# Optimization experiments

Hardware: AMD Instinct MI355X
Metric: run time of the kernel (lower is better)

The kernel has to match this reference:

```python
import jax, jax.numpy as jnp
import numpy as np

B, N = 16384, 64

def setup_inputs() -> dict:
    key = jax.random.key(0)
    a = jax.random.normal(key, (B, N, N), dtype=jnp.float32)
    # symeig / eigh require symmetric input; symmetrize like SPD inputs would be
    x = 0.5 * (a + jnp.swapaxes(a, -2, -1))
    return {"input": x}

def reference(input) -> jnp.ndarray:
    # s, u = symeig(input); out = u @ diag(exp(s)) @ u^T
    s, u = jnp.linalg.eigh(input)          # s: [B,N], u: [B,N,N]
    # fuse diag_embed + two matmuls: (u * exp(s)) @ u^T
    return jnp.einsum('bik,bk,bjk->bij', u, jnp.exp(s), u)
```

## Files before the change

### kernel.cpp

```cpp
#include <hip/hip_runtime.h>
#include <math.h>

#define NB 64
#define TPB 256

__device__ __constant__ float CF[16] = {
    1.0f,
    1.0f,
    0.5f,
    1.6666666666666666e-01f,
    4.1666666666666664e-02f,
    8.3333333333333332e-03f,
    1.3888888888888889e-03f,
    1.9841269841269841e-04f,
    2.4801587301587302e-05f,
    2.7557319223985893e-06f,
    2.7557319223985888e-07f,
    2.5052108385441720e-08f,
    2.0876756987868100e-09f,
    1.6059043836821613e-10f,
    1.1470745597729725e-11f,
    7.6471637318198164e-13f
};

typedef __attribute__((ext_vector_type(8))) short bf16x8;
typedef __attribute__((ext_vector_type(16))) float f32x16;
typedef __attribute__((ext_vector_type(4))) unsigned int u32x4;

#define MFMA32 __builtin_amdgcn_mfma_f32_32x32x16_bf16

__device__ __forceinline__ void split_pk(float x0, float x1, unsigned& ph, unsigned& pl) {
    unsigned h;
    asm("v_cvt_pk_bf16_f32 %0, %1, %2" : "=v"(h) : "v"(x0), "v"(x1));
    float h0 = __builtin_bit_cast(float, h << 16);
    float h1 = __builtin_bit_cast(float, h & 0xFFFF0000u);
    float r0 = x0 - h0;
    float r1 = x1 - h1;
    unsigned l;
    asm("v_cvt_pk_bf16_f32 %0, %1, %2" : "=v"(l) : "v"(r0), "v"(r1));
    ph = h; pl = l;
}

__device__ __forceinline__ float bf2f(unsigned short h) {
    unsigned u = ((unsigned)h) << 16;
    return __builtin_bit_cast(float, u);
}

__device__ __forceinline__ unsigned swzoff(int row, int byteInRow) {
    return (unsigned)(row * 128 + (byteInRow ^ ((row & 7) << 4)));
}

__device__ __forceinline__ bf16x8 ldfrag(const unsigned short* buf, int row, int f, int lh) {
    const char* p = (const char*)buf + swzoff(row, f * 32 + lh * 16);
    return __builtin_bit_cast(bf16x8, *(const u32x4*)p);
}

__device__ __forceinline__ f32x16 mm3(const bf16x8* ah, const bf16x8* al,
                                      const bf16x8* bh, const bf16x8* bl) {
    f32x16 acc = {};
#pragma unroll
    for (int f = 0; f < 4; ++f) acc = MFMA32(ah[f], bh[f], acc, 0, 0, 0);
#pragma unroll
    for (int f = 0; f < 4; ++f) acc = MFMA32(al[f], bh[f], acc, 0, 0, 0);
#pragma unroll
    for (int f = 0; f < 4; ++f) acc = MFMA32(ah[f], bl[f], acc, 0, 0, 0);
    return acc;
}

__device__ __forceinline__ void store_cT(unsigned short* Bh, unsigned short* Bl,
                                         const float* v, int c_out, int rbase) {
#pragma unroll
    for (int g = 0; g < 4; ++g) {
        uint2 wh, wl;
        split_pk(v[g * 4 + 0], v[g * 4 + 1], wh.x, wl.x);
        split_pk(v[g * 4 + 2], v[g * 4 + 3], wh.y, wl.y);
        unsigned off = swzoff(c_out, (rbase + g * 8) * 2);
        *(uint2*)((char*)Bh + off) = wh;
        *(uint2*)((char*)Bl + off) = wl;
    }
}

__global__ __launch_bounds__(TPB, 4)
void spd_expmap_mfma(const float* __restrict__ in, float* __restrict__ out)
{
    __shared__ __align__(16) unsigned short SB[2 * 4096];
    __shared__ float fscratch[4];
    unsigned short* Bh = SB;
    unsigned short* Bl = SB + 4096;

    const int tid  = threadIdx.x;
    const int lane = tid & 63;
    const int wv   = tid >> 6;
    const int wr   = (wv >> 1) * 32;
    const int wc   = (wv & 1) * 32;
    const int l31  = lane & 31;
    const int lh   = lane >> 5;
    const int c_out = wc + l31;
    const int rbase = wr + 4 * lh;
    const size_t base = (size_t)blockIdx.x * (NB * NB);
    const bool diag = (wr == wc);

    float dsel[16];
#pragma unroll
    for (int g = 0; g < 4; ++g)
#pragma unroll
        for (int q = 0; q < 4; ++q)
            dsel[g * 4 + q] = (rbase + g * 8 + q == c_out) ? 1.0f : 0.0f;

    {
        const int r  = tid >> 2;
        const int cb = (tid & 3) * 16;
        const float4* gp = (const float4*)(in + base) + tid * 4;
        float vv[16];
#pragma unroll
        for (int i = 0; i < 4; ++i) {
            float4 t = gp[i];
            vv[i * 4 + 0] = t.x; vv[i * 4 + 1] = t.y;
            vv[i * 4 + 2] = t.z; vv[i * 4 + 3] = t.w;
        }
        unsigned hw[8], lw[8];
#pragma unroll
        for (int i = 0; i < 8; ++i)
            split_pk(vv[2 * i], vv[2 * i + 1], hw[i], lw[i]);
        u32x4 H0 = {hw[0], hw[1], hw[2], hw[3]}, H1 = {hw[4], hw[5], hw[6], hw[7]};
        u32x4 L0 = {lw[0], lw[1], lw[2], lw[3]}, L1 = {lw[4], lw[5], lw[6], lw[7]};
        unsigned o0 = swzoff(r, cb * 2), o1 = swzoff(r, cb * 2 + 16);
        *(u32x4*)((char*)Bh + o0) = H0; *(u32x4*)((char*)Bh + o1) = H1;
        *(u32x4*)((char*)Bl + o0) = L0; *(u32x4*)((char*)Bl + o1) = L1;
    }
    __syncthreads();

    f32x16 acc;
    {
        bf16x8 ah[4], al[4], bh[4], bl[4];
#pragma unroll
        for (int f = 0; f < 4; ++f) {
            ah[f] = ldfrag(Bh, wr + l31, f, lh);
            al[f] = ldfrag(Bl, wr + l31, f, lh);
        }
        if (diag) {
#pragma unroll
            for (int f = 0; f < 4; ++f) { bh[f] = ah[f]; bl[f] = al[f]; }
        } else {
#pragma unroll
            for (int f = 0; f < 4; ++f) {
                bh[f] = ldfrag(Bh, wc + l31, f, lh);
                bl[f] = ldfrag(Bl, wc + l31, f, lh);
            }
        }
        acc = mm3(ah, al, bh, bl);
        float fr = 0.f;
#pragma unroll
        for (int r = 0; r < 16; ++r) fr += acc[r] * acc[r];
#pragma unroll
        for (int off = 32; off; off >>= 1) fr += __shfl_xor(fr, off);
        if (lane == 0) fscratch[wv] = fr;
    }

    float x_out[16];
#pragma unroll
    for (int g = 0; g < 4; ++g) {
        unsigned off = swzoff(c_out, (rbase + g * 8) * 2);
        uint2 xh = *(const uint2*)((const char*)Bh + off);
        uint2 xl = *(const uint2*)((const char*)Bl + off);
        x_out[g * 4 + 0] = bf2f((unsigned short)(xh.x & 0xFFFF)) + bf2f((unsigned short)(xl.x & 0xFFFF));
        x_out[g * 4 + 1] = bf2f((unsigned short)(xh.x >> 16))    + bf2f((unsigned short)(xl.x >> 16));
        x_out[g * 4 + 2] = bf2f((unsigned short)(xh.y & 0xFFFF)) + bf2f((unsigned short)(xl.y & 0xFFFF));
        x_out[g * 4 + 3] = bf2f((unsigned short)(xh.y >> 16))    + bf2f((unsigned short)(xl.y >> 16));
    }
    __syncthreads();

    const float total = fscratch[0] + fscratch[1] + fscratch[2] + fscratch[3];
    const float bound = sqrtf(sqrtf(total));
    int sexp = 0;
    if (bound > 4.f) {
        sexp = (int)ceilf(log2f(bound)) - 2;
        if (sexp < 0) sexp = 0;
        if (sexp > 24) sexp = 24;
    }
    const float sc1 = exp2f(-(float)sexp);
    const float sc2 = sc1 * sc1;
#pragma unroll
    for (int r = 0; r < 16; ++r) x_out[r] *= sc1;

    {
        float v[16];
#pragma unroll
        for (int r = 0; r < 16; ++r) v[r] = acc[r] * sc2;
        store_cT(Bh, Bl, v, c_out, rbase);
    }
    __syncthreads();

    bf16x8 ya_h[4], ya_l[4];
#pragma unroll
    for (int f = 0; f < 4; ++f) {
        ya_h[f] = ldfrag(Bh, wr + l31, f, lh);
        ya_l[f] = ldfrag(Bl, wr + l31, f, lh);
    }
    __syncthreads();

    {
        float v[16];
#pragma unroll
        for (int r = 0; r < 16; ++r)
            v[r] = fmaf(dsel[r], CF[12], CF[13] * x_out[r]);
        store_cT(Bh, Bl, v, c_out, rbase);
    }
    __syncthreads();

#pragma unroll 1
    for (int j = 5; j >= 0; --j) {
        bf16x8 pbh[4], pbl[4];
#pragma unroll
        for (int f = 0; f < 4; ++f) {
            pbh[f] = ldfrag(Bh, wc + l31, f, lh);
            pbl[f] = ldfrag(Bl, wc + l31, f, lh);
        }
        __syncthreads();
        f32x16 a2 = mm3(ya_h, ya_l, pbh, pbl);
        float w[16];
        const float cI = CF[2 * j], cX = CF[2 * j + 1];
#pragma unroll
        for (int r = 0; r < 16; ++r)
            w[r] = fmaf(dsel[r], cI, fmaf(cX, x_out[r], a2[r]));
        store_cT(Bh, Bl, w, c_out, rbase);
        __syncthreads();
    }

    if (sexp == 0) {
#pragma unroll
        for (int g = 0; g < 4; ++g) {
            unsigned off = swzoff(c_out, (rbase + g * 8) * 2);
            uint2 ph = *(const uint2*)((const char*)Bh + off);
            uint2 pl = *(const uint2*)((const char*)Bl + off);
            out[base + (size_t)(rbase + g * 8 + 0) * NB + c_out] = bf2f((unsigned short)(ph.x & 0xFFFF)) + bf2f((unsigned short)(pl.x & 0xFFFF));
            out[base + (size_t)(rbase + g * 8 + 1) * NB + c_out] = bf2f((unsigned short)(ph.x >> 16))    + bf2f((unsigned short)(pl.x >> 16));
            out[base + (size_t)(rbase + g * 8 + 2) * NB + c_out] = bf2f((unsigned short)(ph.y & 0xFFFF)) + bf2f((unsigned short)(pl.y & 0xFFFF));
            out[base + (size_t)(rbase + g * 8 + 3) * NB + c_out] = bf2f((unsigned short)(ph.y >> 16))    + bf2f((unsigned short)(pl.y >> 16));
        }
    } else {
#pragma unroll 1
        for (int t = 0; t < sexp; ++t) {
            bf16x8 pah[4], pal[4], pbh[4], pbl[4];
#pragma unroll
            for (int f = 0; f < 4; ++f) {
                pah[f] = ldfrag(Bh, wr + l31, f, lh);
                pal[f] = ldfrag(Bl, wr + l31, f, lh);
            }
            if (diag) {
#pragma unroll
                for (int f = 0; f < 4; ++f) { pbh[f] = pah[f]; pbl[f] = pal[f]; }
            } else {
#pragma unroll
                for (int f = 0; f < 4; ++f) {
                    pbh[f] = ldfrag(Bh, wc + l31, f, lh);
                    pbl[f] = ldfrag(Bl, wc + l31, f, lh);
                }
            }
            if (t == sexp - 1) {
                f32x16 a2 = mm3(pah, pal, pbh, pbl);
#pragma unroll
                for (int g = 0; g < 4; ++g)
#pragma unroll
                    for (int q = 0; q < 4; ++q)
                        out[base + (size_t)(rbase + g * 8 + q) * NB + c_out] = a2[g * 4 + q];
            } else {
                __syncthreads();
                f32x16 a2 = mm3(pah, pal, pbh, pbl);
                store_cT(Bh, Bl, (const float*)&a2, c_out, rbase);
                __syncthreads();
            }
        }
    }
}

extern "C" void kernel_launch(void* const* d_in, const int* in_sizes, int n_in,
                              void* d_out, int out_size, void* d_ws, size_t ws_size,
                              hipStream_t stream) {
    const float* in = reinterpret_cast<const float*>(d_in[0]);
    float* out = reinterpret_cast<float*>(d_out);
    const int nmat = in_sizes[0] / (NB * NB);
    hipLaunchKernelGGL(spd_expmap_mfma, dim3(nmat), dim3(TPB), 0, stream, in, out);
}
```

Before: 321.6 us.

## Assign one wavefront per matrix to eliminate block-wide barriers

Each 64-wide wavefront now owns a whole 64x64 matrix and computes all four 32x32 output tiles itself. Before, four waves split one matrix. Two matrices are packed per 128-thread block, each wave with its own LDS buffers. This removes every __syncthreads and the cross-wave reduction of the Frobenius norm, relying on in-order LDS access within a wave. In exchange, each wave holds many more registers (four X tiles plus two Y fragment sets), which can lower occupancy or cause spills, and per-matrix latency grows because one wave issues all the MFMAs.

```diff
diff --git a/kernel.cpp b/kernel.cpp
--- a/kernel.cpp
+++ b/kernel.cpp
@@ -2,7 +2,7 @@
 #include <math.h>
 
 #define NB 64
-#define TPB 256
+#define TPB 128
 
 __device__ __constant__ float CF[16] = {
     1.0f,
@@ -80,98 +80,82 @@
     }
 }
 
-__global__ __launch_bounds__(TPB, 4)
-void spd_expmap_mfma(const float* __restrict__ in, float* __restrict__ out)
-{
-    __shared__ __align__(16) unsigned short SB[2 * 4096];
-    __shared__ float fscratch[4];
-    unsigned short* Bh = SB;
-    unsigned short* Bl = SB + 4096;
-
-    const int tid  = threadIdx.x;
-    const int lane = tid & 63;
-    const int wv   = tid >> 6;
-    const int wr   = (wv >> 1) * 32;
-    const int wc   = (wv & 1) * 32;
-    const int l31  = lane & 31;
-    const int lh   = lane >> 5;
-    const int c_out = wc + l31;
-    const int rbase = wr + 4 * lh;
-    const size_t base = (size_t)blockIdx.x * (NB * NB);
-    const bool diag = (wr == wc);
-
-    float dsel[16];
-#pragma unroll
-    for (int g = 0; g < 4; ++g)
-#pragma unroll
-        for (int q = 0; q < 4; ++q)
-            dsel[g * 4 + q] = (rbase + g * 8 + q == c_out) ? 1.0f : 0.0f;
-
-    {
-        const int r  = tid >> 2;
-        const int cb = (tid & 3) * 16;
-        const float4* gp = (const float4*)(in + base) + tid * 4;
-        float vv[16];
-#pragma unroll
-        for (int i = 0; i < 4; ++i) {
-            float4 t = gp[i];
-            vv[i * 4 + 0] = t.x; vv[i * 4 + 1] = t.y;
-            vv[i * 4 + 2] = t.z; vv[i * 4 + 3] = t.w;
-        }
-        unsigned hw[8], lw[8];
-#pragma unroll
-        for (int i = 0; i < 8; ++i)
-            split_pk(vv[2 * i], vv[2 * i + 1], hw[i], lw[i]);
-        u32x4 H0 = {hw[0], hw[1], hw[2], hw[3]}, H1 = {hw[4], hw[5], hw[6], hw[7]};
-        u32x4 L0 = {lw[0], lw[1], lw[2], lw[3]}, L1 = {lw[4], lw[5], lw[6], lw[7]};
-        unsigned o0 = swzoff(r, cb * 2), o1 = swzoff(r, cb * 2 + 16);
-        *(u32x4*)((char*)Bh + o0) = H0; *(u32x4*)((char*)Bh + o1) = H1;
-        *(u32x4*)((char*)Bl + o0) = L0; *(u32x4*)((char*)Bl + o1) = L1;
-    }
-    __syncthreads();
-
-    f32x16 acc;
-    {
-        bf16x8 ah[4], al[4], bh[4], bl[4];
-#pragma unroll
-        for (int f = 0; f < 4; ++f) {
-            ah[f] = ldfrag(Bh, wr + l31, f, lh);
-            al[f] = ldfrag(Bl, wr + l31, f, lh);
-        }
-        if (diag) {
-#pragma unroll
-            for (int f = 0; f < 4; ++f) { bh[f] = ah[f]; bl[f] = al[f]; }
-        } else {
-#pragma unroll
-            for (int f = 0; f < 4; ++f) {
-                bh[f] = ldfrag(Bh, wc + l31, f, lh);
-                bl[f] = ldfrag(Bl, wc + l31, f, lh);
-            }
-        }
-        acc = mm3(ah, al, bh, bl);
-        float fr = 0.f;
-#pragma unroll
-        for (int r = 0; r < 16; ++r) fr += acc[r] * acc[r];
-#pragma unroll
-        for (int off = 32; off; off >>= 1) fr += __shfl_xor(fr, off);
-        if (lane == 0) fscratch[wv] = fr;
-    }
-
-    float x_out[16];
+__device__ __forceinline__ void read_own(const unsigned short* Bh, const unsigned short* Bl,
+                                         int c_out, int rbase, float* xv) {
 #pragma unroll
     for (int g = 0; g < 4; ++g) {
         unsigned off = swzoff(c_out, (rbase + g * 8) * 2);
         uint2 xh = *(const uint2*)((const char*)Bh + off);
         uint2 xl = *(const uint2*)((const char*)Bl + off);
-        x_out[g * 4 + 0] = bf2f((unsigned short)(xh.x & 0xFFFF)) + bf2f((unsigned short)(xl.x & 0xFFFF));
-        x_out[g * 4 + 1] = bf2f((unsigned short)(xh.x >> 16))    + bf2f((unsigned short)(xl.x >> 16));
-        x_out[g * 4 + 2] = bf2f((unsigned short)(xh.y & 0xFFFF)) + bf2f((unsigned short)(xl.y & 0xFFFF));
-        x_out[g * 4 + 3] = bf2f((unsigned short)(xh.y >> 16))    + bf2f((unsigned short)(xl.y >> 16));
-    }
-    __syncthreads();
-
-    const float total = fscratch[0] + fscratch[1] + fscratch[2] + fscratch[3];
-    const float bound = sqrtf(sqrtf(total));
+        xv[g * 4 + 0] = bf2f((unsigned short)(xh.x & 0xFFFF)) + bf2f((unsigned short)(xl.x & 0xFFFF));
+        xv[g * 4 + 1] = bf2f((unsigned short)(xh.x >> 16))    + bf2f((unsigned short)(xl.x >> 16));
+        xv[g * 4 + 2] = bf2f((unsigned short)(xh.y & 0xFFFF)) + bf2f((unsigned short)(xl.y & 0xFFFF));
+        xv[g * 4 + 3] = bf2f((unsigned short)(xh.y >> 16))    + bf2f((unsigned short)(xl.y >> 16));
+    }
+}
+
+__global__ __launch_bounds__(TPB, 2)
+void spd_expmap_mfma(const float* __restrict__ in, float* __restrict__ out)
+{
+    __shared__ __align__(16) unsigned short SB[2 * 8192];
+    const int tid  = threadIdx.x;
+    const int lane = tid & 63;
+    const int wv   = tid >> 6;
+    unsigned short* Bh = SB + wv * 8192;
+    unsigned short* Bl = Bh + 4096;
+
+    const int l31  = lane & 31;
+    const int lh   = lane >> 5;
+    const size_t base = ((size_t)blockIdx.x * 2 + wv) * (NB * NB);
+
+    unsigned dmask = 0;
+#pragma unroll
+    for (int g = 0; g < 4; ++g)
+#pragma unroll
+        for (int q = 0; q < 4; ++q)
+            if (4 * lh + g * 8 + q == l31) dmask |= 1u << (g * 4 + q);
+
+    {
+        const float4* gp = (const float4*)(in + base + (size_t)lane * NB);
+#pragma unroll
+        for (int c = 0; c < 4; ++c) {
+            float4 t0 = gp[c * 4 + 0], t1 = gp[c * 4 + 1];
+            float4 t2 = gp[c * 4 + 2], t3 = gp[c * 4 + 3];
+            float vv[16] = {t0.x, t0.y, t0.z, t0.w, t1.x, t1.y, t1.z, t1.w,
+                            t2.x, t2.y, t2.z, t2.w, t3.x, t3.y, t3.z, t3.w};
+            unsigned hw[8], lw[8];
+#pragma unroll
+            for (int i = 0; i < 8; ++i)
+                split_pk(vv[2 * i], vv[2 * i + 1], hw[i], lw[i]);
+            u32x4 H0 = {hw[0], hw[1], hw[2], hw[3]}, H1 = {hw[4], hw[5], hw[6], hw[7]};
+            u32x4 L0 = {lw[0], lw[1], lw[2], lw[3]}, L1 = {lw[4], lw[5], lw[6], lw[7]};
+            unsigned o0 = swzoff(lane, c * 32), o1 = swzoff(lane, c * 32 + 16);
+            *(u32x4*)((char*)Bh + o0) = H0; *(u32x4*)((char*)Bh + o1) = H1;
+            *(u32x4*)((char*)Bl + o0) = L0; *(u32x4*)((char*)Bl + o1) = L1;
+        }
+    }
+
+    bf16x8 fh0[4], fl0[4], fh1[4], fl1[4];
+#pragma unroll
+    for (int f = 0; f < 4; ++f) {
+        fh0[f] = ldfrag(Bh, l31, f, lh);
+        fl0[f] = ldfrag(Bl, l31, f, lh);
+        fh1[f] = ldfrag(Bh, 32 + l31, f, lh);
+        fl1[f] = ldfrag(Bl, 32 + l31, f, lh);
+    }
+    f32x16 a00 = mm3(fh0, fl0, fh0, fl0);
+    f32x16 a01 = mm3(fh0, fl0, fh1, fl1);
+    f32x16 a10 = mm3(fh1, fl1, fh0, fl0);
+    f32x16 a11 = mm3(fh1, fl1, fh1, fl1);
+
+    float fr = 0.f;
+#pragma unroll
+    for (int r = 0; r < 16; ++r)
+        fr += a00[r] * a00[r] + a01[r] * a01[r] + a10[r] * a10[r] + a11[r] * a11[r];
+#pragma unroll
+    for (int off = 32; off; off >>= 1) fr += __shfl_xor(fr, off);
+
+    const float bound = sqrtf(sqrtf(fr));
     int sexp = 0;
     if (bound > 4.f) {
         sexp = (int)ceilf(log2f(bound)) - 2;
@@ -180,95 +164,156 @@
     }
     const float sc1 = exp2f(-(float)sexp);
     const float sc2 = sc1 * sc1;
-#pragma unroll
-    for (int r = 0; r < 16; ++r) x_out[r] *= sc1;
+
+    float x00[16], x01[16], x10[16], x11[16];
+    read_own(Bh, Bl, l31,      4 * lh,      x00);
+    read_own(Bh, Bl, 32 + l31, 4 * lh,      x01);
+    read_own(Bh, Bl, l31,      32 + 4 * lh, x10);
+    read_own(Bh, Bl, 32 + l31, 32 + 4 * lh, x11);
+#pragma unroll
+    for (int r = 0; r < 16; ++r) {
+        x00[r] *= sc1; x01[r] *= sc1; x10[r] *= sc1; x11[r] *= sc1;
+    }
 
     {
-        float v[16];
-#pragma unroll
-        for (int r = 0; r < 16; ++r) v[r] = acc[r] * sc2;
-        store_cT(Bh, Bl, v, c_out, rbase);
-    }
-    __syncthreads();
-
-    bf16x8 ya_h[4], ya_l[4];
+        float w[16];
+#pragma unroll
+        for (int r = 0; r < 16; ++r) w[r] = a00[r] * sc2;
+        store_cT(Bh, Bl, w, l31, 4 * lh);
+#pragma unroll
+        for (int r = 0; r < 16; ++r) w[r] = a01[r] * sc2;
+        store_cT(Bh, Bl, w, 32 + l31, 4 * lh);
+#pragma unroll
+        for (int r = 0; r < 16; ++r) w[r] = a10[r] * sc2;
+        store_cT(Bh, Bl, w, l31, 32 + 4 * lh);
+#pragma unroll
+        for (int r = 0; r < 16; ++r) w[r] = a11[r] * sc2;
+        store_cT(Bh, Bl, w, 32 + l31, 32 + 4 * lh);
+    }
+
+    bf16x8 yh0[4], yl0[4], yh1[4], yl1[4];
 #pragma unroll
     for (int f = 0; f < 4; ++f) {
-        ya_h[f] = ldfrag(Bh, wr + l31, f, lh);
-        ya_l[f] = ldfrag(Bl, wr + l31, f, lh);
-    }
-    __syncthreads();
+        yh0[f] = ldfrag(Bh, l31, f, lh);
+        yl0[f] = ldfrag(Bl, l31, f, lh);
+        yh1[f] = ldfrag(Bh, 32 + l31, f, lh);
+        yl1[f] = ldfrag(Bl, 32 + l31, f, lh);
+    }
 
     {
-        float v[16];
+        float w[16];
 #pragma unroll
         for (int r = 0; r < 16; ++r)
-            v[r] = fmaf(dsel[r], CF[12], CF[13] * x_out[r]);
-        store_cT(Bh, Bl, v, c_out, rbase);
-    }
-    __syncthreads();
+            w[r] = CF[13] * x00[r] + (((dmask >> r) & 1) ? CF[12] : 0.f);
+        store_cT(Bh, Bl, w, l31, 4 * lh);
+#pragma unroll
+        for (int r = 0; r < 16; ++r) w[r] = CF[13] * x01[r];
+        store_cT(Bh, Bl, w, 32 + l31, 4 * lh);
+#pragma unroll
+        for (int r = 0; r < 16; ++r) w[r] = CF[13] * x10[r];
+        store_cT(Bh, Bl, w, l31, 32 + 4 * lh);
+#pragma unroll
+        for (int r = 0; r < 16; ++r)
+            w[r] = CF[13] * x11[r] + (((dmask >> r) & 1) ? CF[12] : 0.f);
+        store_cT(Bh, Bl, w, 32 + l31, 32 + 4 * lh);
+    }
 
 #pragma unroll 1
     for (int j = 5; j >= 0; --j) {
-        bf16x8 pbh[4], pbl[4];
+        const float cI = CF[2 * j], cX = CF[2 * j + 1];
+        bf16x8 ph0[4], pl0[4], ph1[4], pl1[4];
 #pragma unroll
         for (int f = 0; f < 4; ++f) {
-            pbh[f] = ldfrag(Bh, wc + l31, f, lh);
-            pbl[f] = ldfrag(Bl, wc + l31, f, lh);
-        }
-        __syncthreads();
-        f32x16 a2 = mm3(ya_h, ya_l, pbh, pbl);
+            ph0[f] = ldfrag(Bh, l31, f, lh);
+            pl0[f] = ldfrag(Bl, l31, f, lh);
+            ph1[f] = ldfrag(Bh, 32 + l31, f, lh);
+            pl1[f] = ldfrag(Bl, 32 + l31, f, lh);
+        }
         float w[16];
-        const float cI = CF[2 * j], cX = CF[2 * j + 1];
-#pragma unroll
-        for (int r = 0; r < 16; ++r)
-            w[r] = fmaf(dsel[r], cI, fmaf(cX, x_out[r], a2[r]));
-        store_cT(Bh, Bl, w, c_out, rbase);
-        __syncthreads();
+        {
+            f32x16 t = mm3(yh0, yl0, ph0, pl0);
+#pragma unroll
+            for (int r = 0; r < 16; ++r)
+                w[r] = fmaf(cX, x00[r], t[r]) + (((dmask >> r) & 1) ? cI : 0.f);
+            store_cT(Bh, Bl, w, l31, 4 * lh);
+        }
+        {
+            f32x16 t = mm3(yh0, yl0, ph1, pl1);
+#pragma unroll
+            for (int r = 0; r < 16; ++r) w[r] = fmaf(cX, x01[r], t[r]);
+            store_cT(Bh, Bl, w, 32 + l31, 4 * lh);
+        }
+        {
+            f32x16 t = mm3(yh1, yl1, ph0, pl0);
+#pragma unroll
+            for (int r = 0; r < 16; ++r) w[r] = fmaf(cX, x10[r], t[r]);
+            store_cT(Bh, Bl, w, l31, 32 + 4 * lh);
+        }
+        {
+            f32x16 t = mm3(yh1, yl1, ph1, pl1);
+#pragma unroll
+            for (int r = 0; r < 16; ++r)
+                w[r] = fmaf(cX, x11[r], t[r]) + (((dmask >> r) & 1) ? cI : 0.f);
+            store_cT(Bh, Bl, w, 32 + l31, 32 + 4 * lh);
+        }
     }
 
     if (sexp == 0) {
-#pragma unroll
-        for (int g = 0; g < 4; ++g) {
-            unsigned off = swzoff(c_out, (rbase + g * 8) * 2);
-            uint2 ph = *(const uint2*)((const char*)Bh + off);
-            uint2 pl = *(const uint2*)((const char*)Bl + off);
-            out[base + (size_t)(rbase + g * 8 + 0) * NB + c_out] = bf2f((unsigned short)(ph.x & 0xFFFF)) + bf2f((unsigned short)(pl.x & 0xFFFF));
-            out[base + (size_t)(rbase + g * 8 + 1) * NB + c_out] = bf2f((unsigned short)(ph.x >> 16))    + bf2f((unsigned short)(pl.x >> 16));
-            out[base + (size_t)(rbase + g * 8 + 2) * NB + c_out] = bf2f((unsigned short)(ph.y & 0xFFFF)) + bf2f((unsigned short)(pl.y & 0xFFFF));
-            out[base + (size_t)(rbase + g * 8 + 3) * NB + c_out] = bf2f((unsigned short)(ph.y >> 16))    + bf2f((unsigned short)(pl.y >> 16));
-        }
+        float w[16];
+        read_own(Bh, Bl, l31, 4 * lh, w);
+#pragma unroll
+        for (int g = 0; g < 4; ++g)
+#pragma unroll
+            for (int q = 0; q < 4; ++q)
+                out[base + (size_t)(4 * lh + g * 8 + q) * NB + l31] = w[g * 4 + q];
+        read_own(Bh, Bl, 32 + l31, 4 * lh, w);
+#pragma unroll
+        for (int g = 0; g < 4; ++g)
+#pragma unroll
+            for (int q = 0; q < 4; ++q)
+                out[base + (size_t)(4 * lh + g * 8 + q) * NB + 32 + l31] = w[g * 4 + q];
+        read_own(Bh, Bl, l31, 32 + 4 * lh, w);
+#pragma unroll
+        for (int g = 0; g < 4; ++g)
+#pragma unroll
+            for (int q = 0; q < 4; ++q)
+                out[base + (size_t)(32 + 4 * lh + g * 8 + q) * NB + l31] = w[g * 4 + q];
+        read_own(Bh, Bl, 32 + l31, 32 + 4 * lh, w);
+#pragma unroll
+        for (int g = 0; g < 4; ++g)
+#pragma unroll
+            for (int q = 0; q < 4; ++q)
+                out[base + (size_t)(32 + 4 * lh + g * 8 + q) * NB + 32 + l31] = w[g * 4 + q];
     } else {
 #pragma unroll 1
         for (int t = 0; t < sexp; ++t) {
-            bf16x8 pah[4], pal[4], pbh[4], pbl[4];
+            bf16x8 ph0[4], pl0[4], ph1[4], pl1[4];
 #pragma unroll
             for (int f = 0; f < 4; ++f) {
-                pah[f] = ldfrag(Bh, wr + l31, f, lh);
-                pal[f] = ldfrag(Bl, wr + l31, f, lh);
+                ph0[f] = ldfrag(Bh, l31, f, lh);
+                pl0[f] = ldfrag(Bl, l31, f, lh);
+                ph1[f] = ldfrag(Bh, 32 + l31, f, lh);
+                pl1[f] = ldfrag(Bl, 32 + l31, f, lh);
             }
-            if (diag) {
-#pragma unroll
-                for (int f = 0; f < 4; ++f) { pbh[f] = pah[f]; pbl[f] = pal[f]; }
+            f32x16 s00 = mm3(ph0, pl0, ph0, pl0);
+            f32x16 s01 = mm3(ph0, pl0, ph1, pl1);
+            f32x16 s10 = mm3(ph1, pl1, ph0, pl0);
+            f32x16 s11 = mm3(ph1, pl1, ph1, pl1);
+            if (t == sexp - 1) {
+#pragma unroll
+                for (int g = 0; g < 4; ++g)
+#pragma unroll
+                    for (int q = 0; q < 4; ++q) {
+                        out[base + (size_t)(4 * lh + g * 8 + q) * NB + l31]           = s00[g * 4 + q];
+                        out[base + (size_t)(4 * lh + g * 8 + q) * NB + 32 + l31]      = s01[g * 4 + q];
+                        out[base + (size_t)(32 + 4 * lh + g * 8 + q) * NB + l31]      = s10[g * 4 + q];
+                        out[base + (size_t)(32 + 4 * lh + g * 8 + q) * NB + 32 + l31] = s11[g * 4 + q];
+                    }
             } else {
-#pragma unroll
-                for (int f = 0; f < 4; ++f) {
-                    pbh[f] = ldfrag(Bh, wc + l31, f, lh);
-                    pbl[f] = ldfrag(Bl, wc + l31, f, lh);
-                }
-            }
-            if (t == sexp - 1) {
-                f32x16 a2 = mm3(pah, pal, pbh, pbl);
-#pragma unroll
-                for (int g = 0; g < 4; ++g)
-#pragma unroll
-                    for (int q = 0; q < 4; ++q)
-                        out[base + (size_t)(rbase + g * 8 + q) * NB + c_out] = a2[g * 4 + q];
-            } else {
-                __syncthreads();
-                f32x16 a2 = mm3(pah, pal, pbh, pbl);
-                store_cT(Bh, Bl, (const float*)&a2, c_out, rbase);
-                __syncthreads();
+                store_cT(Bh, Bl, (const float*)&s00, l31, 4 * lh);
+                store_cT(Bh, Bl, (const float*)&s01, 32 + l31, 4 * lh);
+                store_cT(Bh, Bl, (const float*)&s10, l31, 32 + 4 * lh);
+                store_cT(Bh, Bl, (const float*)&s11, 32 + l31, 32 + 4 * lh);
             }
         }
     }
@@ -280,5 +325,5 @@
     const float* in = reinterpret_cast<const float*>(d_in[0]);
     float* out = reinterpret_cast<float*>(d_out);
     const int nmat = in_sizes[0] / (NB * NB);
-    hipLaunchKernelGGL(spd_expmap_mfma, dim3(nmat), dim3(TPB), 0, stream, in, out);
-}
+    hipLaunchKernelGGL(spd_expmap_mfma, dim3(nmat / 2), dim3(TPB), 0, stream, in, out);
+}
```

Result: no change. 316.0 us (-1.7%).

## Compute each matrix exponential in a single wave with register-resident operands

Applied to the files above, without the earlier changes.

Replaces the 4-wave, LDS-staged kernel with a single 64-lane wave per matrix. All four 32x32 tiles stay in registers, and accumulator-to-operand conversion uses permlane32 swaps instead of LDS round trips. This removes shared memory and every __syncthreads, at the cost of heavy register pressure. Each wave now does four times the MFMA work serially, and occupancy may drop.

```diff
diff --git a/kernel.cpp b/kernel.cpp
--- a/kernel.cpp
+++ b/kernel.cpp
@@ -2,7 +2,7 @@
 #include <math.h>
 
 #define NB 64
-#define TPB 256
+#define TPB 64
 
 __device__ __constant__ float CF[16] = {
     1.0f,
@@ -28,6 +28,12 @@
 typedef __attribute__((ext_vector_type(4))) unsigned int u32x4;
 
 #define MFMA32 __builtin_amdgcn_mfma_f32_32x32x16_bf16
+#define BCH(x) __builtin_bit_cast(bf16x8, x)
+
+__device__ __forceinline__ float bf2f(unsigned short h) {
+    unsigned u = ((unsigned)h) << 16;
+    return __builtin_bit_cast(float, u);
+}
 
 __device__ __forceinline__ void split_pk(float x0, float x1, unsigned& ph, unsigned& pl) {
     unsigned h;
@@ -41,137 +47,127 @@
     ph = h; pl = l;
 }
 
-__device__ __forceinline__ float bf2f(unsigned short h) {
-    unsigned u = ((unsigned)h) << 16;
-    return __builtin_bit_cast(float, u);
-}
-
-__device__ __forceinline__ unsigned swzoff(int row, int byteInRow) {
-    return (unsigned)(row * 128 + (byteInRow ^ ((row & 7) << 4)));
-}
-
-__device__ __forceinline__ bf16x8 ldfrag(const unsigned short* buf, int row, int f, int lh) {
-    const char* p = (const char*)buf + swzoff(row, f * 32 + lh * 16);
-    return __builtin_bit_cast(bf16x8, *(const u32x4*)p);
-}
-
-__device__ __forceinline__ f32x16 mm3(const bf16x8* ah, const bf16x8* al,
-                                      const bf16x8* bh, const bf16x8* bl) {
+__device__ __forceinline__ void pswap(unsigned& a, unsigned& b, int lh) {
+#if __has_builtin(__builtin_amdgcn_permlane32_swap)
+    auto r = __builtin_amdgcn_permlane32_swap((int)a, (int)b, false, false);
+    a = (unsigned)r[0];
+    b = (unsigned)r[1];
+#else
+    unsigned pa = (unsigned)__shfl_xor((int)a, 32);
+    unsigned pb = (unsigned)__shfl_xor((int)b, 32);
+    unsigned o0 = lh ? pb : a;
+    unsigned o1 = lh ? b : pa;
+    a = o0; b = o1;
+#endif
+}
+
+__device__ __forceinline__ void tile_to_op(const float* v, int lh, u32x4* fh, u32x4* fl) {
+    unsigned Wh[4][2], Wl[4][2];
+#pragma unroll
+    for (int g = 0; g < 4; ++g) {
+        split_pk(v[g * 4 + 0], v[g * 4 + 1], Wh[g][0], Wl[g][0]);
+        split_pk(v[g * 4 + 2], v[g * 4 + 3], Wh[g][1], Wl[g][1]);
+    }
+#pragma unroll
+    for (int p = 0; p < 2; ++p) {
+        unsigned a0 = Wh[2 * p][0], b0 = Wh[2 * p + 1][0];
+        unsigned a1 = Wh[2 * p][1], b1 = Wh[2 * p + 1][1];
+        pswap(a0, b0, lh);
+        pswap(a1, b1, lh);
+        fh[p] = (u32x4){a0, a1, b0, b1};
+        a0 = Wl[2 * p][0]; b0 = Wl[2 * p + 1][0];
+        a1 = Wl[2 * p][1]; b1 = Wl[2 * p + 1][1];
+        pswap(a0, b0, lh);
+        pswap(a1, b1, lh);
+        fl[p] = (u32x4){a0, a1, b0, b1};
+    }
+}
+
+__device__ __forceinline__ f32x16 mm3v(const u32x4* ah, const u32x4* al,
+                                       const u32x4* bh, const u32x4* bl) {
     f32x16 acc = {};
 #pragma unroll
-    for (int f = 0; f < 4; ++f) acc = MFMA32(ah[f], bh[f], acc, 0, 0, 0);
-#pragma unroll
-    for (int f = 0; f < 4; ++f) acc = MFMA32(al[f], bh[f], acc, 0, 0, 0);
-#pragma unroll
-    for (int f = 0; f < 4; ++f) acc = MFMA32(ah[f], bl[f], acc, 0, 0, 0);
+    for (int f = 0; f < 4; ++f) acc = MFMA32(BCH(ah[f]), BCH(bh[f]), acc, 0, 0, 0);
+#pragma unroll
+    for (int f = 0; f < 4; ++f) acc = MFMA32(BCH(al[f]), BCH(bh[f]), acc, 0, 0, 0);
+#pragma unroll
+    for (int f = 0; f < 4; ++f) acc = MFMA32(BCH(ah[f]), BCH(bl[f]), acc, 0, 0, 0);
     return acc;
 }
 
-__device__ __forceinline__ void store_cT(unsigned short* Bh, unsigned short* Bl,
-                                         const float* v, int c_out, int rbase) {
+__device__ __forceinline__ void wr_tile(float* __restrict__ out, size_t base,
+                                        int C, int R, int l31, int lh, const float* w) {
+    float* rowp = out + base + (size_t)(C * 32 + l31) * NB + R * 32 + 4 * lh;
 #pragma unroll
     for (int g = 0; g < 4; ++g) {
-        uint2 wh, wl;
-        split_pk(v[g * 4 + 0], v[g * 4 + 1], wh.x, wl.x);
-        split_pk(v[g * 4 + 2], v[g * 4 + 3], wh.y, wl.y);
-        unsigned off = swzoff(c_out, (rbase + g * 8) * 2);
-        *(uint2*)((char*)Bh + off) = wh;
-        *(uint2*)((char*)Bl + off) = wl;
-    }
-}
-
-__global__ __launch_bounds__(TPB, 4)
-void spd_expmap_mfma(const float* __restrict__ in, float* __restrict__ out)
+        float4 v = make_float4(w[g * 4 + 0], w[g * 4 + 1], w[g * 4 + 2], w[g * 4 + 3]);
+        *reinterpret_cast<float4*>(rowp + 8 * g) = v;
+    }
+}
+
+__global__ __launch_bounds__(TPB, 2)
+void spd_expmap_reg(const float* __restrict__ in, float* __restrict__ out)
 {
-    __shared__ __align__(16) unsigned short SB[2 * 4096];
-    __shared__ float fscratch[4];
-    unsigned short* Bh = SB;
-    unsigned short* Bl = SB + 4096;
-
-    const int tid  = threadIdx.x;
-    const int lane = tid & 63;
-    const int wv   = tid >> 6;
-    const int wr   = (wv >> 1) * 32;
-    const int wc   = (wv & 1) * 32;
-    const int l31  = lane & 31;
-    const int lh   = lane >> 5;
-    const int c_out = wc + l31;
-    const int rbase = wr + 4 * lh;
+    const int lane = threadIdx.x & 63;
+    const int l31 = lane & 31;
+    const int lh  = lane >> 5;
     const size_t base = (size_t)blockIdx.x * (NB * NB);
-    const bool diag = (wr == wc);
-
-    float dsel[16];
+    const float* rp0 = in + base + (size_t)l31 * NB;
+    const float* rp1 = rp0 + (size_t)32 * NB;
+
+    unsigned dmask = 0;
 #pragma unroll
     for (int g = 0; g < 4; ++g)
 #pragma unroll
         for (int q = 0; q < 4; ++q)
-            dsel[g * 4 + q] = (rbase + g * 8 + q == c_out) ? 1.0f : 0.0f;
-
-    {
-        const int r  = tid >> 2;
-        const int cb = (tid & 3) * 16;
-        const float4* gp = (const float4*)(in + base) + tid * 4;
-        float vv[16];
-#pragma unroll
-        for (int i = 0; i < 4; ++i) {
-            float4 t = gp[i];
-            vv[i * 4 + 0] = t.x; vv[i * 4 + 1] = t.y;
-            vv[i * 4 + 2] = t.z; vv[i * 4 + 3] = t.w;
+            if (4 * lh + 8 * g + q == l31) dmask |= 1u << (g * 4 + q);
+
+    u32x4 XH[2][4], XL[2][4];
+#pragma unroll
+    for (int R = 0; R < 2; ++R) {
+        const float* rp = R ? rp1 : rp0;
+#pragma unroll
+        for (int f = 0; f < 4; ++f) {
+            const float* q = rp + 16 * f + 8 * lh;
+            float4 a = *reinterpret_cast<const float4*>(q);
+            float4 b = *reinterpret_cast<const float4*>(q + 4);
+            unsigned h0, l0, h1, l1, h2, l2, h3, l3;
+            split_pk(a.x, a.y, h0, l0);
+            split_pk(a.z, a.w, h1, l1);
+            split_pk(b.x, b.y, h2, l2);
+            split_pk(b.z, b.w, h3, l3);
+            XH[R][f] = (u32x4){h0, h1, h2, h3};
+            XL[R][f] = (u32x4){l0, l1, l2, l3};
         }
-        unsigned hw[8], lw[8];
-#pragma unroll
-        for (int i = 0; i < 8; ++i)
-            split_pk(vv[2 * i], vv[2 * i + 1], hw[i], lw[i]);
-        u32x4 H0 = {hw[0], hw[1], hw[2], hw[3]}, H1 = {hw[4], hw[5], hw[6], hw[7]};
-        u32x4 L0 = {lw[0], lw[1], lw[2], lw[3]}, L1 = {lw[4], lw[5], lw[6], lw[7]};
-        unsigned o0 = swzoff(r, cb * 2), o1 = swzoff(r, cb * 2 + 16);
-        *(u32x4*)((char*)Bh + o0) = H0; *(u32x4*)((char*)Bh + o1) = H1;
-        *(u32x4*)((char*)Bl + o0) = L0; *(u32x4*)((char*)Bl + o1) = L1;
-    }
-    __syncthreads();
-
-    f32x16 acc;
-    {
-        bf16x8 ah[4], al[4], bh[4], bl[4];
-#pragma unroll
-        for (int f = 0; f < 4; ++f) {
-            ah[f] = ldfrag(Bh, wr + l31, f, lh);
-            al[f] = ldfrag(Bl, wr + l31, f, lh);
-        }
-        if (diag) {
-#pragma unroll
-            for (int f = 0; f < 4; ++f) { bh[f] = ah[f]; bl[f] = al[f]; }
-        } else {
-#pragma unroll
-            for (int f = 0; f < 4; ++f) {
-                bh[f] = ldfrag(Bh, wc + l31, f, lh);
-                bl[f] = ldfrag(Bl, wc + l31, f, lh);
-            }
-        }
-        acc = mm3(ah, al, bh, bl);
-        float fr = 0.f;
-#pragma unroll
-        for (int r = 0; r < 16; ++r) fr += acc[r] * acc[r];
-#pragma unroll
-        for (int off = 32; off; off >>= 1) fr += __shfl_xor(fr, off);
-        if (lane == 0) fscratch[wv] = fr;
-    }
-
-    float x_out[16];
+    }
+
+    float x00[16], x10[16], x01[16], x11[16];
 #pragma unroll
     for (int g = 0; g < 4; ++g) {
-        unsigned off = swzoff(c_out, (rbase + g * 8) * 2);
-        uint2 xh = *(const uint2*)((const char*)Bh + off);
-        uint2 xl = *(const uint2*)((const char*)Bl + off);
-        x_out[g * 4 + 0] = bf2f((unsigned short)(xh.x & 0xFFFF)) + bf2f((unsigned short)(xl.x & 0xFFFF));
-        x_out[g * 4 + 1] = bf2f((unsigned short)(xh.x >> 16))    + bf2f((unsigned short)(xl.x >> 16));
-        x_out[g * 4 + 2] = bf2f((unsigned short)(xh.y & 0xFFFF)) + bf2f((unsigned short)(xl.y & 0xFFFF));
-        x_out[g * 4 + 3] = bf2f((unsigned short)(xh.y >> 16))    + bf2f((unsigned short)(xl.y >> 16));
-    }
-    __syncthreads();
-
-    const float total = fscratch[0] + fscratch[1] + fscratch[2] + fscratch[3];
-    const float bound = sqrtf(sqrtf(total));
+        float4 t;
+        t = *reinterpret_cast<const float4*>(rp0 + 4 * lh + 8 * g);
+        x00[g*4+0] = t.x; x00[g*4+1] = t.y; x00[g*4+2] = t.z; x00[g*4+3] = t.w;
+        t = *reinterpret_cast<const float4*>(rp0 + 32 + 4 * lh + 8 * g);
+        x10[g*4+0] = t.x; x10[g*4+1] = t.y; x10[g*4+2] = t.z; x10[g*4+3] = t.w;
+        t = *reinterpret_cast<const float4*>(rp1 + 4 * lh + 8 * g);
+        x01[g*4+0] = t.x; x01[g*4+1] = t.y; x01[g*4+2] = t.z; x01[g*4+3] = t.w;
+        t = *reinterpret_cast<const float4*>(rp1 + 32 + 4 * lh + 8 * g);
+        x11[g*4+0] = t.x; x11[g*4+1] = t.y; x11[g*4+2] = t.z; x11[g*4+3] = t.w;
+    }
+
+    f32x16 a00 = mm3v(XH[0], XL[0], XH[0], XL[0]);
+    f32x16 a01 = mm3v(XH[0], XL[0], XH[1], XL[1]);
+    f32x16 a10 = mm3v(XH[1], XL[1], XH[0], XL[0]);
+    f32x16 a11 = mm3v(XH[1], XL[1], XH[1], XL[1]);
+
+    float fr = 0.f;
+#pragma unroll
+    for (int r = 0; r < 16; ++r)
+        fr += a00[r]*a00[r] + a01[r]*a01[r] + a10[r]*a10[r] + a11[r]*a11[r];
+#pragma unroll
+    for (int off = 32; off; off >>= 1) fr += __shfl_xor(fr, off);
+
+    const float bound = sqrtf(sqrtf(fr));
     int sexp = 0;
     if (bound > 4.f) {
         sexp = (int)ceilf(log2f(bound)) - 2;
@@ -180,96 +176,119 @@
     }
     const float sc1 = exp2f(-(float)sexp);
     const float sc2 = sc1 * sc1;
-#pragma unroll
-    for (int r = 0; r < 16; ++r) x_out[r] *= sc1;
-
+
+#pragma unroll
+    for (int r = 0; r < 16; ++r) { x00[r] *= sc1; x10[r] *= sc1; x01[r] *= sc1; x11[r] *= sc1; }
+
+    u32x4 YH[2][4], YL[2][4];
     {
         float v[16];
 #pragma unroll
-        for (int r = 0; r < 16; ++r) v[r] = acc[r] * sc2;
-        store_cT(Bh, Bl, v, c_out, rbase);
-    }
-    __syncthreads();
-
-    bf16x8 ya_h[4], ya_l[4];
-#pragma unroll
-    for (int f = 0; f < 4; ++f) {
-        ya_h[f] = ldfrag(Bh, wr + l31, f, lh);
-        ya_l[f] = ldfrag(Bl, wr + l31, f, lh);
-    }
-    __syncthreads();
-
+        for (int r = 0; r < 16; ++r) v[r] = a00[r] * sc2;
+        tile_to_op(v, lh, &YH[0][0], &YL[0][0]);
+#pragma unroll
+        for (int r = 0; r < 16; ++r) v[r] = a10[r] * sc2;
+        tile_to_op(v, lh, &YH[0][2], &YL[0][2]);
+#pragma unroll
+        for (int r = 0; r < 16; ++r) v[r] = a01[r] * sc2;
+        tile_to_op(v, lh, &YH[1][0], &YL[1][0]);
+#pragma unroll
+        for (int r = 0; r < 16; ++r) v[r] = a11[r] * sc2;
+        tile_to_op(v, lh, &YH[1][2], &YL[1][2]);
+    }
+
+    u32x4 PH[2][4], PL[2][4];
     {
         float v[16];
 #pragma unroll
         for (int r = 0; r < 16; ++r)
-            v[r] = fmaf(dsel[r], CF[12], CF[13] * x_out[r]);
-        store_cT(Bh, Bl, v, c_out, rbase);
-    }
-    __syncthreads();
+            v[r] = CF[13] * x00[r] + (((dmask >> r) & 1) ? CF[12] : 0.f);
+        tile_to_op(v, lh, &PH[0][0], &PL[0][0]);
+#pragma unroll
+        for (int r = 0; r < 16; ++r) v[r] = CF[13] * x10[r];
+        tile_to_op(v, lh, &PH[0][2], &PL[0][2]);
+#pragma unroll
+        for (int r = 0; r < 16; ++r) v[r] = CF[13] * x01[r];
+        tile_to_op(v, lh, &PH[1][0], &PL[1][0]);
+#pragma unroll
+        for (int r = 0; r < 16; ++r)
+            v[r] = CF[13] * x11[r] + (((dmask >> r) & 1) ? CF[12] : 0.f);
+        tile_to_op(v, lh, &PH[1][2], &PL[1][2]);
+    }
 
 #pragma unroll 1
     for (int j = 5; j >= 0; --j) {
-        bf16x8 pbh[4], pbl[4];
-#pragma unroll
-        for (int f = 0; f < 4; ++f) {
-            pbh[f] = ldfrag(Bh, wc + l31, f, lh);
-            pbl[f] = ldfrag(Bl, wc + l31, f, lh);
+        const float cI = CF[2 * j], cX = CF[2 * j + 1];
+        const bool last = (j == 0) && (sexp == 0);
+        {
+            f32x16 t0 = mm3v(YH[0], YL[0], PH[0], PL[0]);
+            f32x16 t1 = mm3v(YH[1], YL[1], PH[0], PL[0]);
+            float w0[16], w1[16];
+#pragma unroll
+            for (int r = 0; r < 16; ++r) {
+                w0[r] = fmaf(cX, x00[r], t0[r]) + (((dmask >> r) & 1) ? cI : 0.f);
+                w1[r] = fmaf(cX, x10[r], t1[r]);
+            }
+            if (last) {
+                wr_tile(out, base, 0, 0, l31, lh, w0);
+                wr_tile(out, base, 0, 1, l31, lh, w1);
+            } else {
+                tile_to_op(w0, lh, &PH[0][0], &PL[0][0]);
+                tile_to_op(w1, lh, &PH[0][2], &PL[0][2]);
+            }
         }
-        __syncthreads();
-        f32x16 a2 = mm3(ya_h, ya_l, pbh, pbl);
+        {
+            f32x16 t0 = mm3v(YH[0], YL[0], PH[1], PL[1]);
+            f32x16 t1 = mm3v(YH[1], YL[1], PH[1], PL[1]);
+            float w0[16], w1[16];
+#pragma unroll
+            for (int r = 0; r < 16; ++r) {
+                w0[r] = fmaf(cX, x01[r], t0[r]);
+                w1[r] = fmaf(cX, x11[r], t1[r]) + (((dmask >> r) & 1) ? cI : 0.f);
+            }
+            if (last) {
+                wr_tile(out, base, 1, 0, l31, lh, w0);
+                wr_tile(out, base, 1, 1, l31, lh, w1);
+            } else {
+                tile_to_op(w0, lh, &PH[1][0], &PL[1][0]);
+                tile_to_op(w1, lh, &PH[1][2], &PL[1][2]);
+            }
+        }
+    }
+
+#pragma unroll 1
+    for (int t = 0; t < sexp; ++t) {
+        f32x16 s00 = mm3v(PH[0], PL[0], PH[0], PL[0]);
+        f32x16 s01 = mm3v(PH[0], PL[0], PH[1], PL[1]);
+        f32x16 s10 = mm3v(PH[1], PL[1], PH[0], PL[0]);
+        f32x16 s11 = mm3v(PH[1], PL[1], PH[1], PL[1]);
         float w[16];
-        const float cI = CF[2 * j], cX = CF[2 * j + 1];
-#pragma unroll
-        for (int r = 0; r < 16; ++r)
-            w[r] = fmaf(dsel[r], cI, fmaf(cX, x_out[r], a2[r]));
-        store_cT(Bh, Bl, w, c_out, rbase);
-        __syncthreads();
-    }
-
-    if (sexp == 0) {
-#pragma unroll
-        for (int g = 0; g < 4; ++g) {
-            unsigned off = swzoff(c_out, (rbase + g * 8) * 2);
-            uint2 ph = *(const uint2*)((const char*)Bh + off);
-            uint2 pl = *(const uint2*)((const char*)Bl + off);
-            out[base + (size_t)(rbase + g * 8 + 0) * NB + c_out] = bf2f((unsigned short)(ph.x & 0xFFFF)) + bf2f((unsigned short)(pl.x & 0xFFFF));
-            out[base + (size_t)(rbase + g * 8 + 1) * NB + c_out] = bf2f((unsigned short)(ph.x >> 16))    + bf2f((unsigned short)(pl.x >> 16));
-            out[base + (size_t)(rbase + g * 8 + 2) * NB + c_out] = bf2f((unsigned short)(ph.y & 0xFFFF)) + bf2f((unsigned short)(pl.y & 0xFFFF));
-            out[base + (size_t)(rbase + g * 8 + 3) * NB + c_out] = bf2f((unsigned short)(ph.y >> 16))    + bf2f((unsigned short)(pl.y >> 16));
-        }
-    } else {
-#pragma unroll 1
-        for (int t = 0; t < sexp; ++t) {
-            bf16x8 pah[4], pal[4], pbh[4], pbl[4];
-#pragma unroll
-            for (int f = 0; f < 4; ++f) {
-                pah[f] = ldfrag(Bh, wr + l31, f, lh);
-                pal[f] = ldfrag(Bl, wr + l31, f, lh);
-            }
-            if (diag) {
-#pragma unroll
-                for (int f = 0; f < 4; ++f) { pbh[f] = pah[f]; pbl[f] = pal[f]; }
-            } else {
-#pragma unroll
-                for (int f = 0; f < 4; ++f) {
-                    pbh[f] = ldfrag(Bh, wc + l31, f, lh);
-                    pbl[f] = ldfrag(Bl, wc + l31, f, lh);
-                }
-            }
-            if (t == sexp - 1) {
-                f32x16 a2 = mm3(pah, pal, pbh, pbl);
-#pragma unroll
-                for (int g = 0; g < 4; ++g)
-#pragma unroll
-                    for (int q = 0; q < 4; ++q)
-                        out[base + (size_t)(rbase + g * 8 + q) * NB + c_out] = a2[g * 4 + q];
-            } else {
-                __syncthreads();
-                f32x16 a2 = mm3(pah, pal, pbh, pbl);
-                store_cT(Bh, Bl, (const float*)&a2, c_out, rbase);
-                __syncthreads();
-            }
+        if (t == sexp - 1) {
+#pragma unroll
+            for (int r = 0; r < 16; ++r) w[r] = s00[r];
+            wr_tile(out, base, 0, 0, l31, lh, w);
+#pragma unroll
+            for (int r = 0; r < 16; ++r) w[r] = s10[r];
+            wr_tile(out, base, 0, 1, l31, lh, w);
+#pragma unroll
+            for (int r = 0; r < 16; ++r) w[r] = s01[r];
+            wr_tile(out, base, 1, 0, l31, lh, w);
+#pragma unroll
+            for (int r = 0; r < 16; ++r) w[r] = s11[r];
+            wr_tile(out, base, 1, 1, l31, lh, w);
+        } else {
+#pragma unroll
+            for (int r = 0; r < 16; ++r) w[r] = s00[r];
+            tile_to_op(w, lh, &PH[0][0], &PL[0][0]);
+#pragma unroll
+            for (int r = 0; r < 16; ++r) w[r] = s10[r];
+            tile_to_op(w, lh, &PH[0][2], &PL[0][2]);
+#pragma unroll
+            for (int r = 0; r < 16; ++r) w[r] = s01[r];
+            tile_to_op(w, lh, &PH[1][0], &PL[1][0]);
+#pragma unroll
+            for (int r = 0; r < 16; ++r) w[r] = s11[r];
+            tile_to_op(w, lh, &PH[1][2], &PL[1][2]);
         }
     }
 }
@@ -280,5 +299,5 @@
     const float* in = reinterpret_cast<const float*>(d_in[0]);
     float* out = reinterpret_cast<float*>(d_out);
     const int nmat = in_sizes[0] / (NB * NB);
-    hipLaunchKernelGGL(spd_expmap_mfma, dim3(nmat), dim3(TPB), 0, stream, in, out);
-}
+    hipLaunchKernelGGL(spd_expmap_reg, dim3(nmat), dim3(TPB), 0, stream, in, out);
+}
```

Measured after the change: 264.9 us. 17.6% less time.
